# Kernel optimization log

Measured on AMD Instinct MI355X. Metric: run time of the kernel, lower is better.

## Reference

```python
import jax, jax.numpy as jnp
import numpy as np

N_NODES = 100000
EMB_DIM = 128
N_PAIRS = 1000000
HIDDEN = 256  # spatial_input_dim = 2 * EMB_DIM


def setup_inputs() -> dict:
    key = jax.random.key(0)
    k1, k2, k3, k4 = jax.random.split(key, 4)
    embs = jax.random.normal(k1, (N_NODES, EMB_DIM), dtype=jnp.float32)
    node_indices = jax.random.randint(k2, (N_PAIRS, 2), 0, N_NODES, dtype=jnp.int64)
    # Glorot-ish small init for the classifier weights
    W1 = jax.random.normal(k3, (2 * EMB_DIM, HIDDEN), dtype=jnp.float32) * (1.0 / np.sqrt(2 * EMB_DIM))
    b1 = jnp.zeros((HIDDEN,), dtype=jnp.float32)
    W2 = jax.random.normal(k4, (HIDDEN, 2), dtype=jnp.float32) * (1.0 / np.sqrt(HIDDEN))
    b2 = jnp.zeros((2,), dtype=jnp.float32)
    return {"spatial_nodes_embs": embs, "node_indices": node_indices,
            "W1": W1, "b1": b1, "W2": W2, "b2": b2}


def reference(spatial_nodes_embs, node_indices, W1, b1, W2, b2):
    # Double gather: embs[node_indices] -> [E, 2, D], flatten -> [E, 2*D]
    x = spatial_nodes_embs[node_indices]                 # [E, 2, D]
    x = x.reshape(x.shape[0], -1)                        # [E, 2*D]
    h = jax.nn.relu(x @ W1 + b1)                         # [E, HIDDEN]
    logits = h @ W2 + b2                                 # [E, 2]
    return logits
```

## Files before the change

kernel.cpp:

```cpp
#include <hip/hip_runtime.h>
#include <hip/hip_bf16.h>
#include <cstdint>
#include <cstddef>

typedef unsigned short u16;
typedef __bf16 bf16x8 __attribute__((ext_vector_type(8)));
typedef u16 ushort8 __attribute__((ext_vector_type(8)));
typedef float f32x4 __attribute__((ext_vector_type(4)));

#define EMB_DIM 128
#define KDIM 256
#define HID 256
#define MTILE 64
#define NBLK 512

static __device__ __forceinline__ u16 f2bf(float f) {
    uint32_t u = __builtin_bit_cast(uint32_t, f);
    u += 0x7fffu + ((u >> 16) & 1u);
    return (u16)(u >> 16);
}

__global__ void prep_w1(const float* __restrict__ W1, u16* __restrict__ w1p) {
    int id = blockIdx.x * blockDim.x + threadIdx.x;
    int j   = id & 7;
    int l   = (id >> 3) & 63;
    int kki = (id >> 9) & 7;
    int ntg = id >> 12;
    int k = kki * 32 + ((l >> 4) * 8) + j;
    int n = ntg * 16 + (l & 15);
    w1p[id] = f2bf(W1[k * HID + n]);
}

__global__ void prep_w2(const float* __restrict__ W2, u16* __restrict__ w2ap) {
    int id = blockIdx.x * blockDim.x + threadIdx.x;
    if (id >= 4096) return;
    int j   = id & 7;
    int l   = (id >> 3) & 63;
    int kki = id >> 9;
    int m = l & 15;
    int g = (l >> 4) & 3;
    int k = kki * 32 + g * 4 + ((j >> 2) << 4) + (j & 3);
    w2ap[id] = (m < 2) ? f2bf(W2[k * 2 + m]) : (u16)0;
}

__global__ void prep_embs(const float* __restrict__ in, u16* __restrict__ out, int n) {
    int id = blockIdx.x * blockDim.x + threadIdx.x;
    size_t base = (size_t)id * 8;
    if (base + 8 <= (size_t)n) {
        float4 f0 = *reinterpret_cast<const float4*>(in + base);
        float4 f1 = *reinterpret_cast<const float4*>(in + base + 4);
        ushort8 h;
        h[0] = f2bf(f0.x); h[1] = f2bf(f0.y); h[2] = f2bf(f0.z); h[3] = f2bf(f0.w);
        h[4] = f2bf(f1.x); h[5] = f2bf(f1.y); h[6] = f2bf(f1.z); h[7] = f2bf(f1.w);
        *reinterpret_cast<ushort8*>(out + base) = h;
    }
}

static __device__ __forceinline__ void gload_lds16(const void* g, void* s) {
    __builtin_amdgcn_global_load_lds(
        (const __attribute__((address_space(1))) unsigned int*)g,
        (__attribute__((address_space(3))) unsigned int*)s, 16, 0, 0);
}

static __device__ __forceinline__ void stage_tile(const u16* __restrict__ embT,
                                                  int vidx, unsigned char* xb,
                                                  int w, int l) {
    const int row_off = l >> 5;
    const int csel    = (l >> 4) & 1;
    const int c       = l & 31;
    #pragma unroll
    for (int i = 0; i < 8; ++i) {
        int n00 = __builtin_amdgcn_readlane(vidx, 4 * i + 0);
        int n01 = __builtin_amdgcn_readlane(vidx, 4 * i + 1);
        int n10 = __builtin_amdgcn_readlane(vidx, 4 * i + 2);
        int n11 = __builtin_amdgcn_readlane(vidx, 4 * i + 3);
        int na   = csel ? n01 : n00;
        int nb   = csel ? n11 : n10;
        int node = row_off ? nb : na;
        int r2   = 2 * i + row_off;
        int glow = (c ^ (r2 & 7)) & 15;
        const u16* src = embT + (size_t)node * 128 + glow * 8;
        gload_lds16(src, xb + (size_t)(w * 16 + 2 * i) * 512);
    }
}

__launch_bounds__(256, 2)
__global__ void edge_mlp_bf3(const u16* __restrict__ embT,
                             const int* __restrict__ nidx,
                             const u16* __restrict__ w1p,
                             const u16* __restrict__ w2ap,
                             const float* __restrict__ b1,
                             const float* __restrict__ b2,
                             float* __restrict__ out,
                             int npairs, int ntiles, int nb) {
    __shared__ __align__(16) unsigned char lds[2 * MTILE * 512 + 4 * MTILE * 2 * 4];
    const int t  = threadIdx.x;
    const int w  = t >> 6;
    const int l  = t & 63;
    const int lg = l >> 4;
    const int lc = l & 15;
    const int gmax = 2 * npairs - 1;

    bf16x8 wf1[4][8];
    #pragma unroll
    for (int ht = 0; ht < 4; ++ht)
        #pragma unroll
        for (int kki = 0; kki < 8; ++kki)
            wf1[ht][kki] = *reinterpret_cast<const bf16x8*>(
                w1p + (size_t)(((w * 4 + ht) * 8 + kki) * 64 + l) * 8);
    float4 b1v[4];
    #pragma unroll
    for (int ht = 0; ht < 4; ++ht)
        b1v[ht] = *reinterpret_cast<const float4*>(b1 + w * 64 + ht * 16 + lg * 4);
    bf16x8 af2[2];
    #pragma unroll
    for (int kk = 0; kk < 2; ++kk)
        af2[kk] = *reinterpret_cast<const bf16x8*>(w2ap + (size_t)((w * 2 + kk) * 64 + l) * 8);
    const float b2c = b2[t & 1];

    const int base0 = lc * 512 + ((lg ^ (lc & 3)) << 4) + (((lc >> 2) & 1) << 6);

    float2* part = reinterpret_cast<float2*>(lds + 2 * MTILE * 512);

    int tile = blockIdx.x;

    {
        int gi = 2 * (tile * 64 + w * 16) + l;
        int v0 = nidx[gi < gmax ? gi : gmax];
        stage_tile(embT, v0, lds, w, l);
    }
    int vnext;
    {
        int gi = 2 * ((tile + nb) * 64 + w * 16) + l;
        vnext = nidx[gi < gmax ? gi : gmax];
    }

    int buf = 0;
    for (; tile < ntiles; tile += nb) {
        __syncthreads();

        const int nxt = tile + nb;
        if (nxt < ntiles)
            stage_tile(embT, vnext, lds + (buf ^ 1) * (MTILE * 512), w, l);
        int vfut;
        {
            int gi = 2 * ((nxt + nb) * 64 + w * 16) + l;
            vfut = nidx[gi < gmax ? gi : gmax];
        }

        const int vbuf = base0 + buf * (MTILE * 512);
        f32x4 acc2[4][4] = {};
        #pragma unroll
        for (int kki = 0; kki < 8; ++kki) {
            const int va = vbuf ^ (kki << 6);
            bf16x8 xf[4];
            #pragma unroll
            for (int et = 0; et < 4; ++et)
                xf[et] = *reinterpret_cast<const bf16x8*>(lds + va + et * 8192);
            #pragma unroll
            for (int ht = 0; ht < 4; ++ht)
                #pragma unroll
                for (int et = 0; et < 4; ++et)
                    acc2[ht][et] = __builtin_amdgcn_mfma_f32_16x16x32_bf16(
                        wf1[ht][kki], xf[et], acc2[ht][et], 0, 0, 0);
        }

        #pragma unroll
        for (int et = 0; et < 4; ++et) {
            uint32_t wd[4][2];
            #pragma unroll
            for (int ht = 0; ht < 4; ++ht) {
                float v0 = fmaxf(acc2[ht][et][0] + b1v[ht].x, 0.0f);
                float v1 = fmaxf(acc2[ht][et][1] + b1v[ht].y, 0.0f);
                float v2 = fmaxf(acc2[ht][et][2] + b1v[ht].z, 0.0f);
                float v3 = fmaxf(acc2[ht][et][3] + b1v[ht].w, 0.0f);
                asm("v_cvt_pk_bf16_f32 %0, %1, %2" : "=v"(wd[ht][0]) : "v"(v0), "v"(v1));
                asm("v_cvt_pk_bf16_f32 %0, %1, %2" : "=v"(wd[ht][1]) : "v"(v2), "v"(v3));
            }
            int4 lo4 = make_int4(wd[0][0], wd[0][1], wd[1][0], wd[1][1]);
            int4 hi4 = make_int4(wd[2][0], wd[2][1], wd[3][0], wd[3][1]);
            f32x4 a3 = {0.0f, 0.0f, 0.0f, 0.0f};
            a3 = __builtin_amdgcn_mfma_f32_16x16x32_bf16(
                af2[0], __builtin_bit_cast(bf16x8, lo4), a3, 0, 0, 0);
            a3 = __builtin_amdgcn_mfma_f32_16x16x32_bf16(
                af2[1], __builtin_bit_cast(bf16x8, hi4), a3, 0, 0, 0);
            if (l < 16)
                part[w * 64 + et * 16 + l] = make_float2(a3[0], a3[1]);
        }

        asm volatile("s_waitcnt lgkmcnt(0)\n\ts_barrier" ::: "memory");

        if (t < 128) {
            const float* pf = reinterpret_cast<const float*>(part);
            float s = b2c + pf[t] + pf[128 + t] + pf[256 + t] + pf[384 + t];
            int m = t >> 1;
            if (tile * 64 + m < npairs)
                out[(size_t)tile * 128 + t] = s;
        }

        vnext = vfut;
        buf ^= 1;
    }
}

__launch_bounds__(256, 2)
__global__ void edge_mlp_f32g(const float* __restrict__ embs,
                              const int* __restrict__ nidx,
                              const u16* __restrict__ w1p,
                              const float* __restrict__ b1,
                              const float* __restrict__ W2,
                              const float* __restrict__ b2,
                              float* __restrict__ out,
                              int npairs) {
    __shared__ __align__(16) unsigned char lds[MTILE * 512 + 4 * MTILE * 2 * 4];
    const int t  = threadIdx.x;
    const int e0 = blockIdx.x * MTILE;
    {
        const int row = t >> 2;
        const int seg = t & 3;
        const int e = e0 + row;
        if (e < npairs) {
            const int i0 = nidx[2 * e];
            const int i1 = nidx[2 * e + 1];
            const float* src = (seg < 2) ? (embs + (size_t)i0 * EMB_DIM)
                                         : (embs + (size_t)i1 * EMB_DIM);
            const int cbase = (seg & 1) * 64;
            #pragma unroll
            for (int j = 0; j < 8; ++j) {
                const int c = cbase + j * 8;
                float4 f0 = *reinterpret_cast<const float4*>(src + c);
                float4 f1 = *reinterpret_cast<const float4*>(src + c + 4);
                ushort8 h;
                h[0] = f2bf(f0.x); h[1] = f2bf(f0.y);
                h[2] = f2bf(f0.z); h[3] = f2bf(f0.w);
                h[4] = f2bf(f1.x); h[5] = f2bf(f1.y);
                h[6] = f2bf(f1.z); h[7] = f2bf(f1.w);
                int off = row * 512 + (seg * 64 + j * 8) * 2;
                off ^= (row & 7) << 4;
                *reinterpret_cast<ushort8*>(lds + off) = h;
            }
        }
    }
    __syncthreads();
    const int w  = t >> 6;
    const int l  = t & 63;
    const int lg = l >> 4;
    const int lc = l & 15;
    f32x4 acc[4][4] = {};
    #pragma unroll
    for (int kki = 0; kki < 8; ++kki) {
        const int krow = kki * 32 + lg * 8;
        bf16x8 a[4], b[4];
        #pragma unroll
        for (int mt = 0; mt < 4; ++mt) {
            const int row = mt * 16 + lc;
            int off = row * 512 + krow * 2;
            off ^= (row & 7) << 4;
            a[mt] = *reinterpret_cast<const bf16x8*>(lds + off);
        }
        #pragma unroll
        for (int nt = 0; nt < 4; ++nt)
            b[nt] = *reinterpret_cast<const bf16x8*>(
                w1p + (size_t)(((w * 4 + nt) * 8 + kki) * 64 + l) * 8);
        #pragma unroll
        for (int mt = 0; mt < 4; ++mt)
            #pragma unroll
            for (int nt = 0; nt < 4; ++nt)
                acc[mt][nt] = __builtin_amdgcn_mfma_f32_16x16x32_bf16(
                    a[mt], b[nt], acc[mt][nt], 0, 0, 0);
    }
    float p0[4][4] = {}, p1[4][4] = {};
    #pragma unroll
    for (int nt = 0; nt < 4; ++nt) {
        const int n = w * 64 + nt * 16 + lc;
        const float bnv  = b1[n];
        const float w20 = W2[2 * n];
        const float w21 = W2[2 * n + 1];
        #pragma unroll
        for (int mt = 0; mt < 4; ++mt)
            #pragma unroll
            for (int r = 0; r < 4; ++r) {
                float v = fmaxf(acc[mt][nt][r] + bnv, 0.0f);
                p0[mt][r] = fmaf(v, w20, p0[mt][r]);
                p1[mt][r] = fmaf(v, w21, p1[mt][r]);
            }
    }
    #pragma unroll
    for (int mt = 0; mt < 4; ++mt)
        #pragma unroll
        for (int r = 0; r < 4; ++r) {
            float a0 = p0[mt][r], a1 = p1[mt][r];
            #pragma unroll
            for (int mask = 1; mask < 16; mask <<= 1) {
                a0 += __shfl_xor(a0, mask);
                a1 += __shfl_xor(a1, mask);
            }
            p0[mt][r] = a0; p1[mt][r] = a1;
        }
    float* part = reinterpret_cast<float*>(lds + MTILE * 512);
    if (lc == 0) {
        #pragma unroll
        for (int mt = 0; mt < 4; ++mt)
            #pragma unroll
            for (int r = 0; r < 4; ++r) {
                const int m = mt * 16 + lg * 4 + r;
                part[(w * MTILE + m) * 2 + 0] = p0[mt][r];
                part[(w * MTILE + m) * 2 + 1] = p1[mt][r];
            }
    }
    __syncthreads();
    if (t < 2 * MTILE) {
        const int m = t >> 1, c = t & 1;
        if (e0 + m < npairs) {
            float s = b2[c];
            #pragma unroll
            for (int ww = 0; ww < 4; ++ww)
                s += part[(ww * MTILE + m) * 2 + c];
            out[(size_t)(e0 + m) * 2 + c] = s;
        }
    }
}

extern "C" void kernel_launch(void* const* d_in, const int* in_sizes, int n_in,
                              void* d_out, int out_size, void* d_ws, size_t ws_size,
                              hipStream_t stream) {
    const float* embs = (const float*)d_in[0];
    const int*   nidx = (const int*)d_in[1];
    const float* W1   = (const float*)d_in[2];
    const float* b1   = (const float*)d_in[3];
    const float* W2   = (const float*)d_in[4];
    const float* b2   = (const float*)d_in[5];
    float* out = (float*)d_out;

    u16* w1p = (u16*)d_ws;
    prep_w1<<<(KDIM * HID) / 256, 256, 0, stream>>>(W1, w1p);

    const int npairs = in_sizes[1] / 2;
    const int ntiles = (npairs + MTILE - 1) / MTILE;

    const size_t w2_off   = 131072;
    const size_t embT_off = 131072 + 8192;
    const size_t need = embT_off + (size_t)in_sizes[0] * sizeof(u16);
    if (ws_size >= need) {
        u16* w2ap = (u16*)((char*)d_ws + w2_off);
        u16* embT = (u16*)((char*)d_ws + embT_off);
        prep_w2<<<16, 256, 0, stream>>>(W2, w2ap);
        const int nemb = in_sizes[0];
        prep_embs<<<(nemb + 2047) / 2048, 256, 0, stream>>>(embs, embT, nemb);
        const int nb = NBLK < ntiles ? NBLK : ntiles;
        edge_mlp_bf3<<<nb, 256, 0, stream>>>(embT, nidx, w1p, w2ap, b1, b2,
                                             out, npairs, ntiles, nb);
    } else {
        edge_mlp_f32g<<<ntiles, 256, 0, stream>>>(embs, nidx, w1p, b1, W2, b2,
                                                  out, npairs);
    }
}
```

Before: 149.9 us.

## Split hidden dimension across eight waves per block instead of four

The main edge MLP kernel now launches 512 threads (8 waves) per block, and each wave owns 32 hidden units instead of 64. Each wave stages 8 embedding rows rather than 16 and holds half as many W1 fragments in registers, which is meant to cut register pressure and raise the number of waves available to hide gather latency. The final reduction sums eight per-wave partials instead of four, and the second-layer MFMA per tile drops from two to one per wave. In exchange the block has more LDS partial traffic, a wider barrier across eight waves, and a larger shared-memory partial buffer.

```diff
diff --git a/kernel.cpp b/kernel.cpp
--- a/kernel.cpp
+++ b/kernel.cpp
@@ -13,6 +13,10 @@
 #define HID 256
 #define MTILE 64
 #define NBLK 512
+
+#define XB        (2 * MTILE * 512)
+#define PART_OFF  XB
+#define LDS_BYTES (XB + 4096)
 
 static __device__ __forceinline__ u16 f2bf(float f) {
     uint32_t u = __builtin_bit_cast(uint32_t, f);
@@ -62,14 +66,14 @@
         (__attribute__((address_space(3))) unsigned int*)s, 16, 0, 0);
 }
 
-static __device__ __forceinline__ void stage_tile(const u16* __restrict__ embT,
-                                                  int vidx, unsigned char* xb,
-                                                  int w, int l) {
+static __device__ __forceinline__ void stage_tile8(const u16* __restrict__ embT,
+                                                   int vidx, unsigned char* xb,
+                                                   int w, int l) {
     const int row_off = l >> 5;
     const int csel    = (l >> 4) & 1;
     const int c       = l & 31;
     #pragma unroll
-    for (int i = 0; i < 8; ++i) {
+    for (int i = 0; i < 4; ++i) {
         int n00 = __builtin_amdgcn_readlane(vidx, 4 * i + 0);
         int n01 = __builtin_amdgcn_readlane(vidx, 4 * i + 1);
         int n10 = __builtin_amdgcn_readlane(vidx, 4 * i + 2);
@@ -80,12 +84,12 @@
         int r2   = 2 * i + row_off;
         int glow = (c ^ (r2 & 7)) & 15;
         const u16* src = embT + (size_t)node * 128 + glow * 8;
-        gload_lds16(src, xb + (size_t)(w * 16 + 2 * i) * 512);
-    }
-}
-
-__launch_bounds__(256, 2)
-__global__ void edge_mlp_bf3(const u16* __restrict__ embT,
+        gload_lds16(src, xb + (size_t)(w * 8 + 2 * i) * 512);
+    }
+}
+
+__launch_bounds__(512, 4)
+__global__ void edge_mlp_bf7(const u16* __restrict__ embT,
                              const int* __restrict__ nidx,
                              const u16* __restrict__ w1p,
                              const u16* __restrict__ w2ap,
@@ -93,7 +97,7 @@
                              const float* __restrict__ b2,
                              float* __restrict__ out,
                              int npairs, int ntiles, int nb) {
-    __shared__ __align__(16) unsigned char lds[2 * MTILE * 512 + 4 * MTILE * 2 * 4];
+    __shared__ __align__(16) unsigned char lds[LDS_BYTES];
     const int t  = threadIdx.x;
     const int w  = t >> 6;
     const int l  = t & 63;
@@ -101,37 +105,41 @@
     const int lc = l & 15;
     const int gmax = 2 * npairs - 1;
 
-    bf16x8 wf1[4][8];
-    #pragma unroll
-    for (int ht = 0; ht < 4; ++ht)
+    bf16x8 wf1[2][8];
+    #pragma unroll
+    for (int ht = 0; ht < 2; ++ht)
         #pragma unroll
         for (int kki = 0; kki < 8; ++kki)
             wf1[ht][kki] = *reinterpret_cast<const bf16x8*>(
-                w1p + (size_t)(((w * 4 + ht) * 8 + kki) * 64 + l) * 8);
-    float4 b1v[4];
-    #pragma unroll
-    for (int ht = 0; ht < 4; ++ht)
-        b1v[ht] = *reinterpret_cast<const float4*>(b1 + w * 64 + ht * 16 + lg * 4);
-    bf16x8 af2[2];
-    #pragma unroll
-    for (int kk = 0; kk < 2; ++kk)
-        af2[kk] = *reinterpret_cast<const bf16x8*>(w2ap + (size_t)((w * 2 + kk) * 64 + l) * 8);
-    const float b2c = b2[t & 1];
+                w1p + (size_t)(((w * 2 + ht) * 8 + kki) * 64 + l) * 8);
+    #pragma unroll
+    for (int ht = 0; ht < 2; ++ht)
+        #pragma unroll
+        for (int kki = 0; kki < 8; ++kki)
+            asm volatile("" : "+v"(wf1[ht][kki]));
+
+    bf16x8 af2 = *reinterpret_cast<const bf16x8*>(w2ap + (size_t)(w * 64 + l) * 8);
+    asm volatile("" : "+v"(af2));
+    f32x4 b1v0 = *reinterpret_cast<const f32x4*>(b1 + w * 32 + lg * 4);
+    f32x4 b1v1 = *reinterpret_cast<const f32x4*>(b1 + w * 32 + 16 + lg * 4);
+    asm volatile("" : "+v"(b1v0));
+    asm volatile("" : "+v"(b1v1));
+    float b2c = b2[t & 1];
+    asm volatile("" : "+v"(b2c));
 
     const int base0 = lc * 512 + ((lg ^ (lc & 3)) << 4) + (((lc >> 2) & 1) << 6);
-
-    float2* part = reinterpret_cast<float2*>(lds + 2 * MTILE * 512);
+    float2* part = reinterpret_cast<float2*>(lds + PART_OFF);
 
     int tile = blockIdx.x;
 
     {
-        int gi = 2 * (tile * 64 + w * 16) + l;
+        int gi = 2 * (tile * 64 + w * 8) + l;
         int v0 = nidx[gi < gmax ? gi : gmax];
-        stage_tile(embT, v0, lds, w, l);
+        stage_tile8(embT, v0, lds, w, l);
     }
     int vnext;
     {
-        int gi = 2 * ((tile + nb) * 64 + w * 16) + l;
+        int gi = 2 * ((tile + nb) * 64 + w * 8) + l;
         vnext = nidx[gi < gmax ? gi : gmax];
     }
 
@@ -141,15 +149,15 @@
 
         const int nxt = tile + nb;
         if (nxt < ntiles)
-            stage_tile(embT, vnext, lds + (buf ^ 1) * (MTILE * 512), w, l);
+            stage_tile8(embT, vnext, lds + (buf ^ 1) * (MTILE * 512), w, l);
         int vfut;
         {
-            int gi = 2 * ((nxt + nb) * 64 + w * 16) + l;
+            int gi = 2 * ((nxt + nb) * 64 + w * 8) + l;
             vfut = nidx[gi < gmax ? gi : gmax];
         }
 
         const int vbuf = base0 + buf * (MTILE * 512);
-        f32x4 acc2[4][4] = {};
+        f32x4 acc2[2][4] = {};
         #pragma unroll
         for (int kki = 0; kki < 8; ++kki) {
             const int va = vbuf ^ (kki << 6);
@@ -158,7 +166,7 @@
             for (int et = 0; et < 4; ++et)
                 xf[et] = *reinterpret_cast<const bf16x8*>(lds + va + et * 8192);
             #pragma unroll
-            for (int ht = 0; ht < 4; ++ht)
+            for (int ht = 0; ht < 2; ++ht)
                 #pragma unroll
                 for (int et = 0; et < 4; ++et)
                     acc2[ht][et] = __builtin_amdgcn_mfma_f32_16x16x32_bf16(
@@ -167,23 +175,21 @@
 
         #pragma unroll
         for (int et = 0; et < 4; ++et) {
-            uint32_t wd[4][2];
-            #pragma unroll
-            for (int ht = 0; ht < 4; ++ht) {
-                float v0 = fmaxf(acc2[ht][et][0] + b1v[ht].x, 0.0f);
-                float v1 = fmaxf(acc2[ht][et][1] + b1v[ht].y, 0.0f);
-                float v2 = fmaxf(acc2[ht][et][2] + b1v[ht].z, 0.0f);
-                float v3 = fmaxf(acc2[ht][et][3] + b1v[ht].w, 0.0f);
+            uint32_t wd[2][2];
+            #pragma unroll
+            for (int ht = 0; ht < 2; ++ht) {
+                const f32x4 bv = ht ? b1v1 : b1v0;
+                float v0 = fmaxf(acc2[ht][et][0] + bv[0], 0.0f);
+                float v1 = fmaxf(acc2[ht][et][1] + bv[1], 0.0f);
+                float v2 = fmaxf(acc2[ht][et][2] + bv[2], 0.0f);
+                float v3 = fmaxf(acc2[ht][et][3] + bv[3], 0.0f);
                 asm("v_cvt_pk_bf16_f32 %0, %1, %2" : "=v"(wd[ht][0]) : "v"(v0), "v"(v1));
                 asm("v_cvt_pk_bf16_f32 %0, %1, %2" : "=v"(wd[ht][1]) : "v"(v2), "v"(v3));
             }
             int4 lo4 = make_int4(wd[0][0], wd[0][1], wd[1][0], wd[1][1]);
-            int4 hi4 = make_int4(wd[2][0], wd[2][1], wd[3][0], wd[3][1]);
             f32x4 a3 = {0.0f, 0.0f, 0.0f, 0.0f};
             a3 = __builtin_amdgcn_mfma_f32_16x16x32_bf16(
-                af2[0], __builtin_bit_cast(bf16x8, lo4), a3, 0, 0, 0);
-            a3 = __builtin_amdgcn_mfma_f32_16x16x32_bf16(
-                af2[1], __builtin_bit_cast(bf16x8, hi4), a3, 0, 0, 0);
+                af2, __builtin_bit_cast(bf16x8, lo4), a3, 0, 0, 0);
             if (l < 16)
                 part[w * 64 + et * 16 + l] = make_float2(a3[0], a3[1]);
         }
@@ -192,7 +198,10 @@
 
         if (t < 128) {
             const float* pf = reinterpret_cast<const float*>(part);
-            float s = b2c + pf[t] + pf[128 + t] + pf[256 + t] + pf[384 + t];
+            float s = b2c;
+            #pragma unroll
+            for (int ww = 0; ww < 8; ++ww)
+                s += pf[ww * 128 + t];
             int m = t >> 1;
             if (tile * 64 + m < npairs)
                 out[(size_t)tile * 128 + t] = s;
@@ -250,7 +259,7 @@
     #pragma unroll
     for (int kki = 0; kki < 8; ++kki) {
         const int krow = kki * 32 + lg * 8;
-        bf16x8 a[4], b[4];
+        bf16x8 a[4], bb[4];
         #pragma unroll
         for (int mt = 0; mt < 4; ++mt) {
             const int row = mt * 16 + lc;
@@ -260,52 +269,52 @@
         }
         #pragma unroll
         for (int nt = 0; nt < 4; ++nt)
-            b[nt] = *reinterpret_cast<const bf16x8*>(
+            bb[nt] = *reinterpret_cast<const bf16x8*>(
                 w1p + (size_t)(((w * 4 + nt) * 8 + kki) * 64 + l) * 8);
         #pragma unroll
         for (int mt = 0; mt < 4; ++mt)
             #pragma unroll
             for (int nt = 0; nt < 4; ++nt)
                 acc[mt][nt] = __builtin_amdgcn_mfma_f32_16x16x32_bf16(
-                    a[mt], b[nt], acc[mt][nt], 0, 0, 0);
+                    a[mt], bb[nt], acc[mt][nt], 0, 0, 0);
     }
     float p0[4][4] = {}, p1[4][4] = {};
     #pragma unroll
     for (int nt = 0; nt < 4; ++nt) {
         const int n = w * 64 + nt * 16 + lc;
-        const float bnv  = b1[n];
+        const float bnv = b1[n];
         const float w20 = W2[2 * n];
         const float w21 = W2[2 * n + 1];
         #pragma unroll
         for (int mt = 0; mt < 4; ++mt)
             #pragma unroll
-            for (int r = 0; r < 4; ++r) {
-                float v = fmaxf(acc[mt][nt][r] + bnv, 0.0f);
-                p0[mt][r] = fmaf(v, w20, p0[mt][r]);
-                p1[mt][r] = fmaf(v, w21, p1[mt][r]);
+            for (int rr = 0; rr < 4; ++rr) {
+                float v = fmaxf(acc[mt][nt][rr] + bnv, 0.0f);
+                p0[mt][rr] = fmaf(v, w20, p0[mt][rr]);
+                p1[mt][rr] = fmaf(v, w21, p1[mt][rr]);
             }
     }
     #pragma unroll
     for (int mt = 0; mt < 4; ++mt)
         #pragma unroll
-        for (int r = 0; r < 4; ++r) {
-            float a0 = p0[mt][r], a1 = p1[mt][r];
+        for (int rr = 0; rr < 4; ++rr) {
+            float a0 = p0[mt][rr], a1 = p1[mt][rr];
             #pragma unroll
             for (int mask = 1; mask < 16; mask <<= 1) {
                 a0 += __shfl_xor(a0, mask);
                 a1 += __shfl_xor(a1, mask);
             }
-            p0[mt][r] = a0; p1[mt][r] = a1;
+            p0[mt][rr] = a0; p1[mt][rr] = a1;
         }
     float* part = reinterpret_cast<float*>(lds + MTILE * 512);
     if (lc == 0) {
         #pragma unroll
         for (int mt = 0; mt < 4; ++mt)
             #pragma unroll
-            for (int r = 0; r < 4; ++r) {
-                const int m = mt * 16 + lg * 4 + r;
-                part[(w * MTILE + m) * 2 + 0] = p0[mt][r];
-                part[(w * MTILE + m) * 2 + 1] = p1[mt][r];
+            for (int rr = 0; rr < 4; ++rr) {
+                const int m = mt * 16 + lg * 4 + rr;
+                part[(w * MTILE + m) * 2 + 0] = p0[mt][rr];
+                part[(w * MTILE + m) * 2 + 1] = p1[mt][rr];
             }
     }
     __syncthreads();
@@ -332,23 +341,23 @@
     const float* b2   = (const float*)d_in[5];
     float* out = (float*)d_out;
 
+    const int nemb   = in_sizes[0];
+    const int npairs = in_sizes[1] / 2;
+    const int ntiles = (npairs + MTILE - 1) / MTILE;
+
     u16* w1p = (u16*)d_ws;
     prep_w1<<<(KDIM * HID) / 256, 256, 0, stream>>>(W1, w1p);
 
-    const int npairs = in_sizes[1] / 2;
-    const int ntiles = (npairs + MTILE - 1) / MTILE;
-
     const size_t w2_off   = 131072;
     const size_t embT_off = 131072 + 8192;
-    const size_t need = embT_off + (size_t)in_sizes[0] * sizeof(u16);
+    const size_t need = embT_off + (size_t)nemb * 2;
     if (ws_size >= need) {
         u16* w2ap = (u16*)((char*)d_ws + w2_off);
         u16* embT = (u16*)((char*)d_ws + embT_off);
         prep_w2<<<16, 256, 0, stream>>>(W2, w2ap);
-        const int nemb = in_sizes[0];
         prep_embs<<<(nemb + 2047) / 2048, 256, 0, stream>>>(embs, embT, nemb);
         const int nb = NBLK < ntiles ? NBLK : ntiles;
-        edge_mlp_bf3<<<nb, 256, 0, stream>>>(embT, nidx, w1p, w2ap, b1, b2,
+        edge_mlp_bf7<<<nb, 512, 0, stream>>>(embT, nidx, w1p, w2ap, b1, b2,
                                              out, npairs, ntiles, nb);
     } else {
         edge_mlp_f32g<<<ntiles, 256, 0, stream>>>(embs, nidx, w1p, b1, W2, b2,
```

New measurement: 158.5 us. 1.06x slower.
